# Kernel tuning notes

Measured on AMD Instinct MI355X. Metric: run time of the kernel, lower is better.

## Reference

```python
import jax, jax.numpy as jnp
import numpy as np

B, S, D = 8, 1024, 768
H = 12
HD = D // H  # 64
SCALE = 1.0 / (HD ** 0.5)


def setup_inputs() -> dict:
    key = jax.random.key(0)
    ks = jax.random.split(key, 5)
    x = jax.random.normal(ks[0], (B, S, D), dtype=jnp.float32)
    W_qkv = jax.random.normal(ks[1], (D, 3 * D), dtype=jnp.float32) * 0.02
    b_qkv = jax.random.normal(ks[2], (3 * D,), dtype=jnp.float32) * 0.02
    W_proj = jax.random.normal(ks[3], (D, D), dtype=jnp.float32) * 0.02
    b_proj = jax.random.normal(ks[4], (D,), dtype=jnp.float32) * 0.02
    return {"x": x, "W_qkv": W_qkv, "b_qkv": b_qkv, "W_proj": W_proj, "b_proj": b_proj}


def reference(x, W_qkv, b_qkv, W_proj, b_proj):
    b, s, d = x.shape
    # QKV projection: (B, S, 3D) -> (3, B, H, S, HD)
    qkv = x @ W_qkv + b_qkv
    qkv = qkv.reshape(b, s, 3, H, HD).transpose(2, 0, 3, 1, 4)
    q, k, v = qkv[0], qkv[1], qkv[2]
    # scaled dot-product attention (full matrix, as in the original)
    scores = jnp.einsum("bhqd,bhkd->bhqk", q, k) * SCALE
    attn = jax.nn.softmax(scores, axis=-1)
    out = jnp.einsum("bhqk,bhkd->bhqd", attn, v)
    # merge heads: (B, S, D)
    out = out.transpose(0, 2, 1, 3).reshape(b, s, d)
    return out @ W_proj + b_proj
```

## Files before the change

kernel.cpp:

```cpp
#include <hip/hip_runtime.h>
#include <math.h>

typedef __attribute__((ext_vector_type(8))) unsigned short ushortx8;
typedef __attribute__((ext_vector_type(8))) __bf16 bf16x8;
typedef __attribute__((ext_vector_type(4))) float floatx4;
typedef __attribute__((ext_vector_type(16))) float floatx16;

#define NH 12
#define SEQ 1024
#define DM 768
#define HD 64
#define GK 768
#define QK_SCALE 0.18033688011112042f

#define GLDS16(gp, lp) __builtin_amdgcn_global_load_lds( \
    (const __attribute__((address_space(1))) unsigned int*)(const void*)(gp), \
    (__attribute__((address_space(3))) unsigned int*)(lp), 16, 0, 0)

__device__ __forceinline__ unsigned short f2bf(float f) {
    union { float f; unsigned u; } v; v.f = f;
    unsigned r = v.u + 0x7fffu + ((v.u >> 16) & 1u);
    return (unsigned short)(r >> 16);
}

__device__ __forceinline__ unsigned pk2bf(float f0, float f1) {
    union { float f; unsigned u; } a, b; a.f = f0; b.f = f1;
    return ((a.u + 0x8000u) >> 16) | ((b.u + 0x8000u) & 0xffff0000u);
}

__global__ void k_prep(const float* __restrict__ x, unsigned short* __restrict__ x_bf,
                       const float* __restrict__ Wqkv, unsigned short* __restrict__ WqkvT,
                       const float* __restrict__ Wproj, unsigned short* __restrict__ WprojT) {
    __shared__ float tile[32][33];
    int bx = blockIdx.x;
    if (bx < 6144) {
        int i = bx * 256 + threadIdx.x;
        float4 v = ((const float4*)x)[i];
        ushort4 o;
        o.x = f2bf(v.x); o.y = f2bf(v.y); o.z = f2bf(v.z); o.w = f2bf(v.w);
        ((ushort4*)x_bf)[i] = o;
        return;
    }
    const float* in; unsigned short* out; int R, C, c0, r0;
    if (bx < 7872) {
        int t = bx - 6144;
        in = Wqkv; out = WqkvT; R = 768; C = 2304;
        c0 = (t % 72) * 32; r0 = (t / 72) * 32;
    } else {
        int t = bx - 7872;
        in = Wproj; out = WprojT; R = 768; C = 768;
        c0 = (t % 24) * 32; r0 = (t / 24) * 32;
    }
    int tx = threadIdx.x & 31, ty = threadIdx.x >> 5;
#pragma unroll
    for (int i = 0; i < 4; i++)
        tile[ty + 8 * i][tx] = in[(size_t)(r0 + ty + 8 * i) * C + c0 + tx];
    __syncthreads();
#pragma unroll
    for (int i = 0; i < 4; i++)
        out[(size_t)(c0 + ty + 8 * i) * R + r0 + tx] = f2bf(tile[tx][ty + 8 * i]);
}


__device__ __forceinline__ void stage6(const unsigned short* gA, const unsigned short* gB,
                                       unsigned short* lbuf, int w, int k0) {
#pragma unroll
    for (int g = 0; g < 4; g++)
        GLDS16(gA + (size_t)(w * 64 + g * 16) * GK + k0, lbuf + (w * 64 + g * 16) * 32);
#pragma unroll
    for (int g = 0; g < 2; g++)
        GLDS16(gB + (size_t)(w * 32 + g * 16) * GK + k0, lbuf + 8192 + (w * 32 + g * 16) * 32);
}

__device__ __forceinline__ void mfma32(const unsigned short* Ab, const unsigned short* Bb,
                                       int wm, int wn, int l15, int csw,
                                       floatx4 (&acc)[8][4]) {
    bf16x8 af[8], bfr[4];
#pragma unroll
    for (int m = 0; m < 8; m++)
        af[m] = __builtin_bit_cast(bf16x8,
            *(const ushortx8*)&Ab[(wm * 128 + m * 16 + l15) * 32 + csw]);
#pragma unroll
    for (int n = 0; n < 4; n++)
        bfr[n] = __builtin_bit_cast(bf16x8,
            *(const ushortx8*)&Bb[(wn * 64 + n * 16 + l15) * 32 + csw]);
#pragma unroll
    for (int m = 0; m < 8; m++)
#pragma unroll
        for (int n = 0; n < 4; n++)
            acc[m][n] = __builtin_amdgcn_mfma_f32_16x16x32_bf16(af[m], bfr[n], acc[m][n], 0, 0, 0);
}

__device__ __forceinline__ void gemm_mainloop(const unsigned short* __restrict__ A,
                                              const unsigned short* __restrict__ Bt,
                                              unsigned short* smem, int m0, int n0,
                                              int w, int lane, floatx4 (&acc)[8][4]) {
    int quad = lane >> 4, l15 = lane & 15;
    int wm = w >> 1, wn = w & 1;
    int rA = lane >> 2;
    int cSwz = ((lane & 3) ^ ((lane >> 3) & 3)) * 8;
    int csw = (quad ^ ((l15 >> 1) & 3)) * 8;
    const unsigned short* gA = A + (size_t)(m0 + rA) * GK + cSwz;
    const unsigned short* gB = Bt + (size_t)(n0 + rA) * GK + cSwz;

    stage6(gA, gB, smem, w, 0);
    stage6(gA, gB, smem + 12288, w, 32);
    int cb = 0, sb = 2;
#pragma unroll 1
    for (int t = 0; t < 24; t++) {
        if (t < 23) asm volatile("s_waitcnt vmcnt(6)" ::: "memory");
        else        asm volatile("s_waitcnt vmcnt(0)" ::: "memory");
        __builtin_amdgcn_s_barrier();
        asm volatile("" ::: "memory");
        if (t < 22) stage6(gA, gB, smem + sb * 12288, w, (t + 2) * 32);
        const unsigned short* Ab = smem + cb * 12288;
        mfma32(Ab, Ab + 8192, wm, wn, l15, csw, acc);
        cb = (cb == 2) ? 0 : cb + 1;
        sb = (sb == 2) ? 0 : sb + 1;
    }
}

__global__ __launch_bounds__(256, 2) void k_gemm_qkv(
    const unsigned short* __restrict__ A, const unsigned short* __restrict__ Bt,
    const float* __restrict__ bias,
    unsigned short* __restrict__ Qb, unsigned short* __restrict__ Kb,
    unsigned short* __restrict__ Vt) {
    __shared__ unsigned short smem[36864];
    int tid = threadIdx.x;
    int w = tid >> 6, lane = tid & 63;
    int quad = lane >> 4, l15 = lane & 15;
    int wm = w >> 1, wn = w & 1;
    int lin = blockIdx.x;
    int xcd = lin & 7, slot = lin >> 3;
    int mt_i = xcd * 4 + (slot & 3);
    int nt_i = slot >> 2;
    int m0 = mt_i * 256, n0 = nt_i * 128;

    floatx4 acc[8][4] = {};
    gemm_mainloop(A, Bt, smem, m0, n0, w, lane, acc);

    int tsel = nt_i / 6;
    int bb = m0 >> 10;
    int s_base0 = (m0 & 1023) + wm * 128;
    if (tsel < 2) {
        unsigned short* __restrict__ dst = (tsel == 0) ? Qb : Kb;
#pragma unroll
        for (int m = 0; m < 8; m++) {
            int s_base = s_base0 + m * 16 + quad * 4;
#pragma unroll
            for (int n = 0; n < 4; n++) {
                int n_g = n0 + wn * 64 + n * 16 + l15;
                int nloc = n_g - tsel * 768;
                int hh = nloc >> 6, dd = nloc & 63;
                float bv = bias[n_g];
                size_t base = ((size_t)(bb * NH + hh) * SEQ + s_base) * HD + dd;
                if (tsel == 0) {
#pragma unroll
                    for (int rg = 0; rg < 4; rg++)
                        dst[base + (size_t)rg * HD] = f2bf((acc[m][n][rg] + bv) * QK_SCALE);
                } else {
#pragma unroll
                    for (int rg = 0; rg < 4; rg++)
                        dst[base + (size_t)rg * HD] = f2bf(acc[m][n][rg] + bv);
                }
            }
        }
    } else {
        int head0 = (n0 - 1536) >> 6;
        __syncthreads();
#pragma unroll
        for (int m = 0; m < 8; m++) {
#pragma unroll
            for (int n = 0; n < 4; n++) {
                int col = wn * 64 + n * 16 + l15;
                float bv = bias[n0 + col];
                ushort4 pk;
                pk.x = f2bf(acc[m][n][0] + bv);
                pk.y = f2bf(acc[m][n][1] + bv);
                pk.z = f2bf(acc[m][n][2] + bv);
                pk.w = f2bf(acc[m][n][3] + bv);
                *(ushort4*)&smem[col * 264 + wm * 128 + m * 16 + quad * 4] = pk;
            }
        }
        __syncthreads();
        int col = tid >> 1, part = tid & 1;
        int hh = head0 + (col >> 6), dd = col & 63;
        size_t gbase = ((size_t)(bb * NH + hh) * HD + dd) * SEQ + (m0 & 1023) + part * 128;
#pragma unroll
        for (int i = 0; i < 16; i++)
            *(uint4*)&Vt[gbase + i * 8] = *(const uint4*)&smem[col * 264 + part * 128 + i * 8];
    }
}

__global__ __launch_bounds__(256) void k_attn(
    const unsigned short* __restrict__ Qb, const unsigned short* __restrict__ Kb,
    const unsigned short* __restrict__ Vt, unsigned short* __restrict__ attn_out) {
    __shared__ unsigned short Ks[64 * 72];
    __shared__ unsigned short Vts[64 * 72];
    __shared__ unsigned short Pt[4][32 * 72];
    int tid = threadIdx.x;
    int w = tid >> 6, lane = tid & 63;
    int l31 = lane & 31, lh = lane >> 5;
    int lin = blockIdx.x;
    int xcd = lin & 7, slot = lin >> 3;
    int bh = xcd * 12 + (slot >> 3);
    int qt = slot & 7;
    int b = bh / NH, h = bh - b * NH;
    const unsigned short* Qp = Qb + (size_t)bh * SEQ * HD;
    const unsigned short* Kp = Kb + (size_t)bh * SEQ * HD;
    const unsigned short* Vp = Vt + (size_t)bh * HD * SEQ;
    int q0w = qt * 128 + w * 32;
    unsigned short* Ptw = &Pt[w][0];

    bf16x8 qf[4];
#pragma unroll
    for (int ds = 0; ds < 4; ds++)
        qf[ds] = __builtin_bit_cast(bf16x8,
            *(const ushortx8*)&Qp[(size_t)(q0w + l31) * HD + ds * 16 + lh * 8]);

    floatx16 o[2] = {};
    float lsum = 0.f;

    int rr = tid >> 3, cc8 = (tid & 7) * 8;
    uint4 kr0 = *(const uint4*)&Kp[(size_t)rr * HD + cc8];
    uint4 kr1 = *(const uint4*)&Kp[(size_t)(rr + 32) * HD + cc8];
    uint4 vr0 = *(const uint4*)&Vp[(size_t)rr * SEQ + cc8];
    uint4 vr1 = *(const uint4*)&Vp[(size_t)(rr + 32) * SEQ + cc8];

    for (int kb = 0; kb < SEQ; kb += 64) {
        __syncthreads();
        *(uint4*)&Ks[rr * 72 + cc8] = kr0;
        *(uint4*)&Ks[(rr + 32) * 72 + cc8] = kr1;
        *(uint4*)&Vts[rr * 72 + cc8] = vr0;
        *(uint4*)&Vts[(rr + 32) * 72 + cc8] = vr1;
        if (kb + 64 < SEQ) {
            kr0 = *(const uint4*)&Kp[(size_t)(kb + 64 + rr) * HD + cc8];
            kr1 = *(const uint4*)&Kp[(size_t)(kb + 64 + rr + 32) * HD + cc8];
            vr0 = *(const uint4*)&Vp[(size_t)rr * SEQ + kb + 64 + cc8];
            vr1 = *(const uint4*)&Vp[(size_t)(rr + 32) * SEQ + kb + 64 + cc8];
        }
        __syncthreads();

        floatx16 sc[2] = {};
#pragma unroll
        for (int mt = 0; mt < 2; mt++)
#pragma unroll
            for (int ds = 0; ds < 4; ds++) {
                bf16x8 kf = __builtin_bit_cast(bf16x8,
                    *(const ushortx8*)&Ks[(mt * 32 + l31) * 72 + ds * 16 + lh * 8]);
                sc[mt] = __builtin_amdgcn_mfma_f32_32x32x16_bf16(kf, qf[ds], sc[mt], 0, 0, 0);
            }

#pragma unroll
        for (int mt = 0; mt < 2; mt++)
#pragma unroll
            for (int g = 0; g < 4; g++) {
                float p0 = exp2f(sc[mt][g * 4 + 0]);
                float p1 = exp2f(sc[mt][g * 4 + 1]);
                float p2 = exp2f(sc[mt][g * 4 + 2]);
                float p3 = exp2f(sc[mt][g * 4 + 3]);
                lsum += (p0 + p1) + (p2 + p3);
                uint2 pk;
                pk.x = pk2bf(p0, p1);
                pk.y = pk2bf(p2, p3);
                *(uint2*)&Ptw[l31 * 72 + mt * 32 + g * 8 + lh * 4] = pk;
            }

#pragma unroll
        for (int ks = 0; ks < 4; ks++) {
            bf16x8 pf = __builtin_bit_cast(bf16x8,
                *(const ushortx8*)&Ptw[l31 * 72 + ks * 16 + lh * 8]);
#pragma unroll
            for (int mt = 0; mt < 2; mt++) {
                bf16x8 vf = __builtin_bit_cast(bf16x8,
                    *(const ushortx8*)&Vts[(mt * 32 + l31) * 72 + ks * 16 + lh * 8]);
                o[mt] = __builtin_amdgcn_mfma_f32_32x32x16_bf16(vf, pf, o[mt], 0, 0, 0);
            }
        }
    }

    lsum += __shfl_xor(lsum, 32, 64);
    float inv = 1.0f / lsum;

#pragma unroll
    for (int mt = 0; mt < 2; mt++)
#pragma unroll
        for (int g = 0; g < 4; g++) {
            uint2 pk;
            pk.x = pk2bf(o[mt][g * 4 + 0] * inv, o[mt][g * 4 + 1] * inv);
            pk.y = pk2bf(o[mt][g * 4 + 2] * inv, o[mt][g * 4 + 3] * inv);
            *(uint2*)&Ptw[l31 * 72 + mt * 32 + g * 8 + lh * 4] = pk;
        }
#pragma unroll
    for (int pass = 0; pass < 4; pass++) {
        int row = pass * 8 + (lane >> 3);
        int col8 = (lane & 7) * 8;
        uint4 vv = *(const uint4*)&Ptw[row * 72 + col8];
        *(uint4*)&attn_out[(size_t)(b * SEQ + q0w + row) * DM + h * HD + col8] = vv;
    }
}

__global__ __launch_bounds__(256, 2) void k_gemm_proj(
    const unsigned short* __restrict__ A, const unsigned short* __restrict__ Bt,
    const float* __restrict__ bias, float* __restrict__ out) {
    __shared__ unsigned short smem[36864];
    int tid = threadIdx.x;
    int w = tid >> 6, lane = tid & 63;
    int quad = lane >> 4, l15 = lane & 15;
    int wm = w >> 1, wn = w & 1;
    int lin = blockIdx.x;
    int xcd = lin & 7, slot = lin >> 3;
    int mt_i = xcd * 4 + (slot & 3);
    int nt_i = slot >> 2;
    int m0 = mt_i * 256, n0 = nt_i * 128;

    floatx4 acc[8][4] = {};
    gemm_mainloop(A, Bt, smem, m0, n0, w, lane, acc);

#pragma unroll
    for (int m = 0; m < 8; m++) {
        int m_base = m0 + wm * 128 + m * 16 + quad * 4;
#pragma unroll
        for (int n = 0; n < 4; n++) {
            int n_g = n0 + wn * 64 + n * 16 + l15;
            float bv = bias[n_g];
#pragma unroll
            for (int rg = 0; rg < 4; rg++)
                out[(size_t)(m_base + rg) * DM + n_g] = acc[m][n][rg] + bv;
        }
    }
}

extern "C" void kernel_launch(void* const* d_in, const int* in_sizes, int n_in,
                              void* d_out, int out_size, void* d_ws, size_t ws_size,
                              hipStream_t stream) {
    const float* x     = (const float*)d_in[0];
    const float* Wqkv  = (const float*)d_in[1];
    const float* bqkv  = (const float*)d_in[2];
    const float* Wproj = (const float*)d_in[3];
    const float* bproj = (const float*)d_in[4];
    float* out = (float*)d_out;

    char* ws = (char*)d_ws;
    unsigned short* x_bf   = (unsigned short*)(ws);
    unsigned short* WqkvT  = (unsigned short*)(ws + 12582912);
    unsigned short* WprojT = (unsigned short*)(ws + 16121856);
    unsigned short* Qb     = (unsigned short*)(ws + 17301504);
    unsigned short* Kb     = (unsigned short*)(ws + 29884416);
    unsigned short* Vt     = (unsigned short*)(ws + 42467328);
    unsigned short* attn   = (unsigned short*)(ws + 55050240);

    k_prep<<<8448, 256, 0, stream>>>(x, x_bf, Wqkv, WqkvT, Wproj, WprojT);
    k_gemm_qkv<<<576, 256, 0, stream>>>(x_bf, WqkvT, bqkv, Qb, Kb, Vt);
    k_attn<<<768, 256, 0, stream>>>(Qb, Kb, Vt, attn);
    k_gemm_proj<<<192, 256, 0, stream>>>(attn, WprojT, bproj, out);
}
```

Measured before the change: 198.9 us.

## Keep attention probabilities in registers via permlane swap and XOR-swizzle K/V LDS

The attention kernel no longer writes the exponentiated score tile to LDS and reads it back as the MFMA operand. It packs the values to bf16 with v_cvt_pk_bf16_f32 and uses v_permlane32_swap to rearrange them into the B-operand layout directly in registers. The K and V^T LDS tiles drop the 72-element padded stride for a 64-element stride with an XOR swizzle, which shrinks LDS use while aiming to avoid bank conflicts. This removes an LDS round trip per key block, but depends on inline asm lane-exchange semantics being correct, and adds a barrier before the output staging.

```diff
diff --git a/kernel.cpp b/kernel.cpp
--- a/kernel.cpp
+++ b/kernel.cpp
@@ -60,7 +60,6 @@
     for (int i = 0; i < 4; i++)
         out[(size_t)(c0 + ty + 8 * i) * R + r0 + tx] = f2bf(tile[tx][ty + 8 * i]);
 }
-
 
 __device__ __forceinline__ void stage6(const unsigned short* gA, const unsigned short* gB,
                                        unsigned short* lbuf, int w, int k0) {
@@ -195,8 +194,8 @@
 __global__ __launch_bounds__(256) void k_attn(
     const unsigned short* __restrict__ Qb, const unsigned short* __restrict__ Kb,
     const unsigned short* __restrict__ Vt, unsigned short* __restrict__ attn_out) {
-    __shared__ unsigned short Ks[64 * 72];
-    __shared__ unsigned short Vts[64 * 72];
+    __shared__ unsigned short Ks[64 * 64];
+    __shared__ unsigned short Vts[64 * 64];
     __shared__ unsigned short Pt[4][32 * 72];
     int tid = threadIdx.x;
     int w = tid >> 6, lane = tid & 63;
@@ -222,6 +221,8 @@
     float lsum = 0.f;
 
     int rr = tid >> 3, cc8 = (tid & 7) * 8;
+    int cs = cc8 ^ ((rr & 7) * 8);
+    int rsw = (l31 & 7) * 8;
     uint4 kr0 = *(const uint4*)&Kp[(size_t)rr * HD + cc8];
     uint4 kr1 = *(const uint4*)&Kp[(size_t)(rr + 32) * HD + cc8];
     uint4 vr0 = *(const uint4*)&Vp[(size_t)rr * SEQ + cc8];
@@ -229,10 +230,10 @@
 
     for (int kb = 0; kb < SEQ; kb += 64) {
         __syncthreads();
-        *(uint4*)&Ks[rr * 72 + cc8] = kr0;
-        *(uint4*)&Ks[(rr + 32) * 72 + cc8] = kr1;
-        *(uint4*)&Vts[rr * 72 + cc8] = vr0;
-        *(uint4*)&Vts[(rr + 32) * 72 + cc8] = vr1;
+        *(uint4*)&Ks[rr * 64 + cs] = kr0;
+        *(uint4*)&Ks[(rr + 32) * 64 + cs] = kr1;
+        *(uint4*)&Vts[rr * 64 + cs] = vr0;
+        *(uint4*)&Vts[(rr + 32) * 64 + cs] = vr1;
         if (kb + 64 < SEQ) {
             kr0 = *(const uint4*)&Kp[(size_t)(kb + 64 + rr) * HD + cc8];
             kr1 = *(const uint4*)&Kp[(size_t)(kb + 64 + rr + 32) * HD + cc8];
@@ -247,33 +248,43 @@
 #pragma unroll
             for (int ds = 0; ds < 4; ds++) {
                 bf16x8 kf = __builtin_bit_cast(bf16x8,
-                    *(const ushortx8*)&Ks[(mt * 32 + l31) * 72 + ds * 16 + lh * 8]);
+                    *(const ushortx8*)&Ks[(mt * 32 + l31) * 64 + ((ds * 16 + lh * 8) ^ rsw)]);
                 sc[mt] = __builtin_amdgcn_mfma_f32_32x32x16_bf16(kf, qf[ds], sc[mt], 0, 0, 0);
             }
 
-#pragma unroll
-        for (int mt = 0; mt < 2; mt++)
-#pragma unroll
-            for (int g = 0; g < 4; g++) {
-                float p0 = exp2f(sc[mt][g * 4 + 0]);
-                float p1 = exp2f(sc[mt][g * 4 + 1]);
-                float p2 = exp2f(sc[mt][g * 4 + 2]);
-                float p3 = exp2f(sc[mt][g * 4 + 3]);
-                lsum += (p0 + p1) + (p2 + p3);
-                uint2 pk;
-                pk.x = pk2bf(p0, p1);
-                pk.y = pk2bf(p2, p3);
-                *(uint2*)&Ptw[l31 * 72 + mt * 32 + g * 8 + lh * 4] = pk;
-            }
+        float p0[16], p1[16];
+#pragma unroll
+        for (int r = 0; r < 16; r++) {
+            p0[r] = exp2f(sc[0][r]);
+            p1[r] = exp2f(sc[1][r]);
+            lsum += p0[r] + p1[r];
+        }
+
+        uint4 pw[4];
+#pragma unroll
+        for (int mt = 0; mt < 2; mt++) {
+            const float* pp = mt ? p1 : p0;
+#pragma unroll
+            for (int hf = 0; hf < 2; hf++) {
+                unsigned a, bq, c, d;
+                asm("v_cvt_pk_bf16_f32 %0, %1, %2" : "=v"(a)  : "v"(pp[hf * 8 + 0]), "v"(pp[hf * 8 + 1]));
+                asm("v_cvt_pk_bf16_f32 %0, %1, %2" : "=v"(bq) : "v"(pp[hf * 8 + 4]), "v"(pp[hf * 8 + 5]));
+                asm("v_cvt_pk_bf16_f32 %0, %1, %2" : "=v"(c)  : "v"(pp[hf * 8 + 2]), "v"(pp[hf * 8 + 3]));
+                asm("v_cvt_pk_bf16_f32 %0, %1, %2" : "=v"(d)  : "v"(pp[hf * 8 + 6]), "v"(pp[hf * 8 + 7]));
+                asm("v_permlane32_swap_b32 %0, %1" : "+v"(a), "+v"(bq));
+                asm("v_permlane32_swap_b32 %0, %1" : "+v"(c), "+v"(d));
+                uint4 wv; wv.x = a; wv.y = c; wv.z = bq; wv.w = d;
+                pw[mt * 2 + hf] = wv;
+            }
+        }
 
 #pragma unroll
         for (int ks = 0; ks < 4; ks++) {
-            bf16x8 pf = __builtin_bit_cast(bf16x8,
-                *(const ushortx8*)&Ptw[l31 * 72 + ks * 16 + lh * 8]);
+            bf16x8 pf = __builtin_bit_cast(bf16x8, pw[ks]);
 #pragma unroll
             for (int mt = 0; mt < 2; mt++) {
                 bf16x8 vf = __builtin_bit_cast(bf16x8,
-                    *(const ushortx8*)&Vts[(mt * 32 + l31) * 72 + ks * 16 + lh * 8]);
+                    *(const ushortx8*)&Vts[(mt * 32 + l31) * 64 + ((ks * 16 + lh * 8) ^ rsw)]);
                 o[mt] = __builtin_amdgcn_mfma_f32_32x32x16_bf16(vf, pf, o[mt], 0, 0, 0);
             }
         }
@@ -291,6 +302,7 @@
             pk.y = pk2bf(o[mt][g * 4 + 2] * inv, o[mt][g * 4 + 3] * inv);
             *(uint2*)&Ptw[l31 * 72 + mt * 32 + g * 8 + lh * 4] = pk;
         }
+    __builtin_amdgcn_s_barrier();
 #pragma unroll
     for (int pass = 0; pass < 4; pass++) {
         int row = pass * 8 + (lane >> 3);
```

Measured after the change: 193.6 us. 2.7% less time.
